# Optimization experiments

Measured on AMD Instinct MI355X. Metric: run time of the kernel, lower is better.

The kernel has to match this reference:

```python
import jax, jax.numpy as jnp
import numpy as np

V, D, H, L, T_MAX = 95, 384, 6, 6, 256
HD = D // H  # 64
FF = 4 * D


def _layernorm(x, scale, bias, eps=1e-5):
    m = jnp.mean(x, axis=-1, keepdims=True)
    v = jnp.var(x, axis=-1, keepdims=True)
    return (x - m) * jax.lax.rsqrt(v + eps) * scale + bias


def setup_inputs() -> dict:
    key = jax.random.key(0)
    ks = iter(jax.random.split(key, 32))
    std = 0.02
    p = {
        "idx": jax.random.randint(next(ks), (128, 256), 0, V, dtype=jnp.int64)
               if jax.config.jax_enable_x64 else
               jax.random.randint(next(ks), (128, 256), 0, V, dtype=jnp.int32),
        "tok_emb": jax.random.normal(next(ks), (V, D), jnp.float32) * std,
        "pos_emb": jax.random.normal(next(ks), (T_MAX, D), jnp.float32) * std,
        # per-layer stacked params [L, ...]
        "ln1_s": jnp.ones((L, D), jnp.float32),
        "ln1_b": jnp.zeros((L, D), jnp.float32),
        "wq": jax.random.normal(next(ks), (L, D, D), jnp.float32) * std,
        "wk": jax.random.normal(next(ks), (L, D, D), jnp.float32) * std,
        "wv": jax.random.normal(next(ks), (L, D, D), jnp.float32) * std,
        "wo": jax.random.normal(next(ks), (L, D, D), jnp.float32) * std,
        "bo": jnp.zeros((L, D), jnp.float32),
        "ln2_s": jnp.ones((L, D), jnp.float32),
        "ln2_b": jnp.zeros((L, D), jnp.float32),
        "w1": jax.random.normal(next(ks), (L, D, FF), jnp.float32) * std,
        "b1": jnp.zeros((L, FF), jnp.float32),
        "w2": jax.random.normal(next(ks), (L, FF, D), jnp.float32) * std,
        "b2": jnp.zeros((L, D), jnp.float32),
        "lnf_s": jnp.ones((D,), jnp.float32),
        "lnf_b": jnp.zeros((D,), jnp.float32),
        "head_w": jax.random.normal(next(ks), (D, V), jnp.float32) * std,
        "head_b": jnp.zeros((V,), jnp.float32),
    }
    return p


def reference(idx, tok_emb, pos_emb, ln1_s, ln1_b, wq, wk, wv, wo, bo,
              ln2_s, ln2_b, w1, b1, w2, b2, lnf_s, lnf_b, head_w, head_b):
    B, T = idx.shape
    x = tok_emb[idx] + pos_emb[:T]  # [B,T,D]
    mask = jnp.tril(jnp.ones((T, T), bool))  # causal
    scale = HD ** -0.5

    def block(x, p):
        s1, b1n, Wq, Wk, Wv, Wo, Bo, s2, b2n, W1, B1, W2, B2 = p
        h = _layernorm(x, s1, b1n)
        q = (h @ Wq).reshape(B, T, H, HD)
        k = (h @ Wk).reshape(B, T, H, HD)
        v = (h @ Wv).reshape(B, T, H, HD)
        scores = jnp.einsum('bqhd,bkhd->bhqk', q, k) * scale
        scores = jnp.where(mask, scores, -jnp.inf)
        wei = jax.nn.softmax(scores, axis=-1)
        attn = jnp.einsum('bhqk,bkhd->bqhd', wei, v).reshape(B, T, D)
        x = x + attn @ Wo + Bo
        h2 = _layernorm(x, s2, b2n)
        x = x + jax.nn.relu(h2 @ W1 + B1) @ W2 + B2
        return x, None

    x, _ = jax.lax.scan(block, x, (ln1_s, ln1_b, wq, wk, wv, wo, bo,
                                   ln2_s, ln2_b, w1, b1, w2, b2))
    logits = _layernorm(x, lnf_s, lnf_b) @ head_w + head_b  # [B,T,V]
    return logits
```

## Files before the change

kernel.cpp:

```cpp
#include <hip/hip_runtime.h>
#include <hip/hip_bf16.h>
#include <cstdint>

#define DEV __device__ __forceinline__

typedef __hip_bfloat16 bf16;
typedef unsigned short u16;
typedef unsigned int u32;
typedef __attribute__((ext_vector_type(8))) short s8v;
typedef __attribute__((ext_vector_type(4))) float f4;

static constexpr int Bn = 128;
static constexpr int Tn = 256;
static constexpr int Dn = 384;
static constexpr int Hn = 6;
static constexpr int HDn = 64;
static constexpr int FFn = 1536;
static constexpr int Vn = 95;
static constexpr int Mn = Bn * 256;

DEV u16 f2b(float f) {
  bf16 h = __float2bfloat16(f);
  return *reinterpret_cast<u16*>(&h);
}
DEV u32 pk2(float a, float b) { return (u32)f2b(a) | ((u32)f2b(b) << 16); }

DEV void gl_lds16(const void* g, void* l) {
  auto gp = (const __attribute__((address_space(1))) u32*)(uintptr_t)g;
  auto lp = (__attribute__((address_space(3))) u32*)(u32)(uintptr_t)l;
  __builtin_amdgcn_global_load_lds(gp, lp, 16, 0, 0);
}

template <int MODE, bool RELU, int NKT, int NT>
__global__ __launch_bounds__(256) void gemm_h(
    const u16* __restrict__ A, const u16* __restrict__ Bw,
    const float* __restrict__ bias, const float* __restrict__ resid,
    void* __restrict__ outp)
{
  constexpr int K = NKT * 64;
  constexpr int N = NT * 16;
  constexpr int nTiles = NT / 8;
  __shared__ __align__(16) u16 As[2][128 * 64];
  const int tid = threadIdx.x;
  const int lane = tid & 63, wave = tid >> 6;
  const int quad = lane >> 4, l16 = lane & 15;
  const int wy = wave >> 1, wx = wave & 1;
  const int blk = blockIdx.x;
  const int xcd = blk & 7, tt = blk >> 3;
  const int nT = tt % nTiles, mT = xcd + 8 * (tt / nTiles);
  const int mBase = mT * 128, nBase = nT * 128;

  f4 acc[4][4] = {};

  int rS[4], cS[4];
#pragma unroll
  for (int i = 0; i < 4; i++) {
    int s = i * 256 + tid;
    rS[i] = s >> 3;
    cS[i] = ((s & 7) ^ (rS[i] & 7)) * 8;
  }

  const u16* Ab = A + (size_t)mBase * K;
  const u16* Bp = Bw + (size_t)((nBase >> 4) + wx * 4) * 512 + lane * 8;

#define STAGEA(buf, kt)                                                       \
  do {                                                                        \
    _Pragma("unroll")                                                         \
    for (int i = 0; i < 4; i++)                                               \
      gl_lds16(Ab + (size_t)rS[i] * K + (kt) + cS[i],                         \
               &As[buf][(i * 256 + wave * 64) * 8]);                          \
  } while (0)

  STAGEA(0, 0);
  const int nk = NKT;
#pragma unroll
  for (int ik = 0; ik < nk; ik++) {
    const int cur = ik & 1;
    asm volatile("s_barrier" ::: "memory");
    s8v bq[8];
    if (ik + 1 < nk) {
      STAGEA(cur ^ 1, (ik + 1) * 64);
#pragma unroll
      for (int ks = 0; ks < 2; ks++)
#pragma unroll
        for (int j = 0; j < 4; j++)
          bq[ks * 4 + j] = *(const s8v*)(Bp + (size_t)(ik * 2 + ks) * (NT * 512) + j * 512);
      asm volatile("s_waitcnt vmcnt(12)" ::: "memory");
    } else {
#pragma unroll
      for (int ks = 0; ks < 2; ks++)
#pragma unroll
        for (int j = 0; j < 4; j++)
          bq[ks * 4 + j] = *(const s8v*)(Bp + (size_t)(ik * 2 + ks) * (NT * 512) + j * 512);
      asm volatile("s_waitcnt vmcnt(8)" ::: "memory");
    }
    asm volatile("s_barrier" ::: "memory");
#pragma unroll
    for (int ks = 0; ks < 2; ks++) {
      s8v af[4];
#pragma unroll
      for (int i = 0; i < 4; i++) {
        int row = wy * 64 + i * 16 + l16;
        int ch = (ks * 4 + quad) ^ (row & 7);
        af[i] = *(const s8v*)&As[cur][row * 64 + ch * 8];
      }
#pragma unroll
      for (int i = 0; i < 4; i++)
#pragma unroll
        for (int j = 0; j < 4; j++)
          acc[i][j] = __builtin_amdgcn_mfma_f32_16x16x32_bf16(af[i], bq[ks * 4 + j], acc[i][j], 0, 0, 0);
    }
  }
#undef STAGEA

  if (MODE == 0) {
    u16* out = (u16*)outp;
#pragma unroll
    for (int j = 0; j < 4; j++) {
      int n = nBase + wx * 64 + j * 16 + l16;
      float bv = bias ? bias[n] : 0.f;
#pragma unroll
      for (int i = 0; i < 4; i++) {
        int m0 = mBase + wy * 64 + i * 16 + quad * 4;
#pragma unroll
        for (int r = 0; r < 4; r++) {
          float v = acc[i][j][r] + bv;
          if (RELU) v = fmaxf(v, 0.f);
          out[(size_t)(m0 + r) * N + n] = f2b(v);
        }
      }
    }
  } else if (MODE == 1) {
    float* out = (float*)outp;
#pragma unroll
    for (int j = 0; j < 4; j++) {
      int n = nBase + wx * 64 + j * 16 + l16;
      float bv = bias[n];
#pragma unroll
      for (int i = 0; i < 4; i++) {
        int m0 = mBase + wy * 64 + i * 16 + quad * 4;
#pragma unroll
        for (int r = 0; r < 4; r++) {
          int m = m0 + r;
          out[(size_t)m * N + n] = resid[(size_t)m * N + n] + acc[i][j][r] + bv;
        }
      }
    }
  } else if (MODE == 3) {
    float* out = (float*)outp;
#pragma unroll
    for (int j = 0; j < 4; j++) {
      int n = nBase + wx * 64 + j * 16 + l16;
      if (n < Vn) {
        float bv = bias[n];
#pragma unroll
        for (int i = 0; i < 4; i++) {
          int m0 = mBase + wy * 64 + i * 16 + quad * 4;
#pragma unroll
          for (int r = 0; r < 4; r++)
            out[(size_t)(m0 + r) * Vn + n] = acc[i][j][r] + bv;
        }
      }
    }
  } else if (MODE == 4) {
    u16* qb = (u16*)outp;
    u16* kb = qb + (size_t)Mn * 384;
    u16* vb = kb + (size_t)Mn * 384;
#pragma unroll
    for (int j = 0; j < 4; j++) {
      int n = nBase + wx * 64 + j * 16 + l16;
      if (n < 768) {
        u16* dst = (n < 384) ? qb : kb;
        int col = (n < 384) ? n : (n - 384);
#pragma unroll
        for (int i = 0; i < 4; i++) {
          int m0 = mBase + wy * 64 + i * 16 + quad * 4;
#pragma unroll
          for (int r = 0; r < 4; r++)
            dst[(size_t)(m0 + r) * 384 + col] = f2b(acc[i][j][r]);
        }
      } else {
        int n7 = n - 768;
        int hh = n7 >> 6, d = n7 & 63;
#pragma unroll
        for (int i = 0; i < 4; i++) {
          int m0 = mBase + wy * 64 + i * 16 + quad * 4;
          int b = m0 >> 8, t0 = m0 & 255;
          uint2 w;
          w.x = pk2(acc[i][j][0], acc[i][j][1]);
          w.y = pk2(acc[i][j][2], acc[i][j][3]);
          *(uint2*)&vb[((b * Hn + hh) * HDn + d) * Tn + t0] = w;
        }
      }
    }
  }
}

__global__ __launch_bounds__(256) void attn_kernel(
    const u16* __restrict__ q, const u16* __restrict__ k,
    const u16* __restrict__ vT, u16* __restrict__ ao)
{
  __shared__ __align__(16) u16 Ps[4][2][16 * 40];
  const int tid = threadIdx.x, lane = tid & 63, wave = tid >> 6;
  const int quad = lane >> 4, l16 = lane & 15;
  const int c4 = blockIdx.x / 768;
  const int bh = blockIdx.x - c4 * 768;
  const int b = bh / Hn, h = bh % Hn;
  const u16* qg = q + (b * Tn) * Dn + h * HDn;
  const u16* kg = k + (b * Tn) * Dn + h * HDn;
  const u16* vg = vT + bh * (HDn * Tn);
  u16* aog = ao + (b * Tn) * Dn + h * HDn;
  const float c1 = 0.125f * 1.44269504f;

  const int qt = (wave & 2) ? ((wave & 1) ? 15 - c4 : 8 + c4)
                            : ((wave & 1) ? 7 - c4 : c4);
  const int qglob = qt * 16 + l16;

  const s8v qf0 = *(const s8v*)&qg[qglob * Dn + quad * 8];
  const s8v qf1 = *(const s8v*)&qg[qglob * Dn + 32 + quad * 8];

  float lsum = 0.f;
  f4 O[4] = {};

  const int nch = qt / 2 + 1;
  for (int c2 = 0; c2 < nch; c2++) {
    const int kk0 = c2 * 32;
    f4 S0 = {0.f, 0.f, 0.f, 0.f}, S1 = S0;
    {
      s8v kf = *(const s8v*)&kg[(kk0 + l16) * Dn + quad * 8];
      S0 = __builtin_amdgcn_mfma_f32_16x16x32_bf16(kf, qf0, S0, 0, 0, 0);
      kf = *(const s8v*)&kg[(kk0 + l16) * Dn + 32 + quad * 8];
      S0 = __builtin_amdgcn_mfma_f32_16x16x32_bf16(kf, qf1, S0, 0, 0, 0);
    }
    if (kk0 + 16 <= qt * 16) {
      s8v kf = *(const s8v*)&kg[(kk0 + 16 + l16) * Dn + quad * 8];
      S1 = __builtin_amdgcn_mfma_f32_16x16x32_bf16(kf, qf0, S1, 0, 0, 0);
      kf = *(const s8v*)&kg[(kk0 + 16 + l16) * Dn + 32 + quad * 8];
      S1 = __builtin_amdgcn_mfma_f32_16x16x32_bf16(kf, qf1, S1, 0, 0, 0);
    }
    const int kkq = kk0 + quad * 4;
    f4 E0, E1;
#pragma unroll
    for (int r = 0; r < 4; r++) {
      E0[r] = (kkq + r <= qglob) ? exp2f(S0[r] * c1) : 0.f;
      E1[r] = (kkq + 16 + r <= qglob) ? exp2f(S1[r] * c1) : 0.f;
      lsum += E0[r] + E1[r];
    }
    u16* prow = &Ps[wave][c2 & 1][l16 * 40];
    uint2 w0, w1;
    w0.x = pk2(E0[0], E0[1]); w0.y = pk2(E0[2], E0[3]);
    w1.x = pk2(E1[0], E1[1]); w1.y = pk2(E1[2], E1[3]);
    *(uint2*)&prow[quad * 4] = w0;
    *(uint2*)&prow[16 + quad * 4] = w1;
    const s8v pf = *(const s8v*)&prow[quad * 8];
#pragma unroll
    for (int dm = 0; dm < 4; dm++) {
      s8v vf = *(const s8v*)&vg[(dm * 16 + l16) * Tn + kk0 + quad * 8];
      O[dm] = __builtin_amdgcn_mfma_f32_16x16x32_bf16(vf, pf, O[dm], 0, 0, 0);
    }
  }

  lsum += __shfl_xor(lsum, 16);
  lsum += __shfl_xor(lsum, 32);
  const float inv = 1.0f / lsum;
#pragma unroll
  for (int dm = 0; dm < 4; dm++) {
    uint2 w;
    w.x = pk2(O[dm][0] * inv, O[dm][1] * inv);
    w.y = pk2(O[dm][2] * inv, O[dm][3] * inv);
    *(uint2*)&aog[qglob * Dn + dm * 16 + quad * 4] = w;
  }
}

__global__ __launch_bounds__(256) void ln_kernel(
    const float* __restrict__ x, const float* __restrict__ sc,
    const float* __restrict__ bi, u16* __restrict__ out)
{
  int tok = blockIdx.x * 4 + (threadIdx.x >> 6);
  int lane = threadIdx.x & 63;
  const float* xr = x + (size_t)tok * Dn;
  float v[6];
  float s = 0.f, sq = 0.f;
#pragma unroll
  for (int i = 0; i < 6; i++) {
    v[i] = xr[lane + 64 * i];
    s += v[i];
    sq += v[i] * v[i];
  }
#pragma unroll
  for (int o = 1; o < 64; o <<= 1) {
    s += __shfl_xor(s, o);
    sq += __shfl_xor(sq, o);
  }
  float mean = s * (1.f / 384.f);
  float var = sq * (1.f / 384.f) - mean * mean;
  float inv = rsqrtf(var + 1e-5f);
  u16* orow = out + (size_t)tok * Dn;
#pragma unroll
  for (int i = 0; i < 6; i++) {
    int c = lane + 64 * i;
    orow[c] = f2b((v[i] - mean) * inv * sc[c] + bi[c]);
  }
}

__global__ __launch_bounds__(256) void embed_kernel(
    const int* __restrict__ idx, const float* __restrict__ tok,
    const float* __restrict__ pos, float* __restrict__ x)
{
  int i = blockIdx.x * 256 + threadIdx.x;
  int m = i / 96, c = (i - m * 96) * 4;
  int t = m & (Tn - 1);
  const float4 tv = *(const float4*)&tok[idx[m] * Dn + c];
  const float4 pv = *(const float4*)&pos[t * Dn + c];
  float4 r;
  r.x = tv.x + pv.x; r.y = tv.y + pv.y; r.z = tv.z + pv.z; r.w = tv.w + pv.w;
  *(float4*)&x[m * Dn + c] = r;
}

__global__ __launch_bounds__(256) void tcvt_frag(
    const float* __restrict__ src, u16* __restrict__ dst,
    int K, int C, int NTsub, int NTtot, int ntoff, int total)
{
  int t = blockIdx.x * 256 + threadIdx.x;
  if (t >= total) return;
  int j8 = t & 7;
  int lane = (t >> 3) & 63;
  int rest = t >> 9;
  int nt = rest % NTsub;
  int lkc = rest / NTsub;
  int KC = K >> 5;
  int kc = lkc % KC;
  int l = lkc / KC;
  int quad = lane >> 4, l16 = lane & 15;
  int k = kc * 32 + quad * 8 + j8;
  int n = nt * 16 + l16;
  float v = (n < C) ? src[((size_t)l * K + k) * C + n] : 0.f;
  dst[((size_t)(l * KC + kc) * NTtot + ntoff + nt) * 512 + lane * 8 + j8] = f2b(v);
}

extern "C" void kernel_launch(void* const* d_in, const int* in_sizes, int n_in,
                              void* d_out, int out_size, void* d_ws, size_t ws_size,
                              hipStream_t stream)
{
  (void)in_sizes; (void)n_in; (void)out_size;
  const int*   idx     = (const int*)d_in[0];
  const float* tok_emb = (const float*)d_in[1];
  const float* pos_emb = (const float*)d_in[2];
  const float* ln1_s   = (const float*)d_in[3];
  const float* ln1_b   = (const float*)d_in[4];
  const float* wq      = (const float*)d_in[5];
  const float* wk      = (const float*)d_in[6];
  const float* wv      = (const float*)d_in[7];
  const float* wo      = (const float*)d_in[8];
  const float* bo      = (const float*)d_in[9];
  const float* ln2_s   = (const float*)d_in[10];
  const float* ln2_b   = (const float*)d_in[11];
  const float* w1      = (const float*)d_in[12];
  const float* b1      = (const float*)d_in[13];
  const float* w2      = (const float*)d_in[14];
  const float* b2      = (const float*)d_in[15];
  const float* lnf_s   = (const float*)d_in[16];
  const float* lnf_b   = (const float*)d_in[17];
  const float* head_w  = (const float*)d_in[18];
  const float* head_b  = (const float*)d_in[19];
  float* out = (float*)d_out;

  char* ws = (char*)d_ws;
  float* x  = (float*)(ws + 0);
  u16*   h  = (u16*)(ws + 50331648);
  u16*   qb = (u16*)(ws + 75497472);
  u16*   kb = (u16*)(ws + 100663296);
  u16*   vb = (u16*)(ws + 125829120);
  u16*   ab = (u16*)(ws + 150994944);
  u16*   f1 = qb;
  u16* qkvT = (u16*)(ws + 176160768);
  u16* woT  = qkvT + 6 * 442368;
  u16* w1T  = woT + 6 * 147456;
  u16* w2T  = w1T + 6 * 589824;
  u16* hdT  = w2T + 6 * 589824;
  if (ws_size < (size_t)197492736) return;

  int tot = 6 * 384 * 384;
  tcvt_frag<<<(tot + 255) / 256, 256, 0, stream>>>(wq, qkvT, 384, 384, 24, 72, 0, tot);
  tcvt_frag<<<(tot + 255) / 256, 256, 0, stream>>>(wk, qkvT, 384, 384, 24, 72, 24, tot);
  tcvt_frag<<<(tot + 255) / 256, 256, 0, stream>>>(wv, qkvT, 384, 384, 24, 72, 48, tot);
  tcvt_frag<<<(tot + 255) / 256, 256, 0, stream>>>(wo, woT, 384, 384, 24, 24, 0, tot);
  tot = 6 * 384 * 1536;
  tcvt_frag<<<(tot + 255) / 256, 256, 0, stream>>>(w1, w1T, 384, 1536, 96, 96, 0, tot);
  tcvt_frag<<<(tot + 255) / 256, 256, 0, stream>>>(w2, w2T, 1536, 384, 24, 24, 0, tot);
  tot = 384 * 128;
  tcvt_frag<<<(tot + 255) / 256, 256, 0, stream>>>(head_w, hdT, 384, 95, 8, 8, 0, tot);

  embed_kernel<<<(Mn * 96) / 256, 256, 0, stream>>>(idx, tok_emb, pos_emb, x);

  for (int l = 0; l < 6; l++) {
    ln_kernel<<<Mn / 4, 256, 0, stream>>>(x, ln1_s + l * Dn, ln1_b + l * Dn, h);
    gemm_h<4, false, 6, 72><<<2304, 256, 0, stream>>>(h, qkvT + l * 442368, nullptr, nullptr, qb);
    attn_kernel<<<Bn * Hn * 4, 256, 0, stream>>>(qb, kb, vb, ab);
    gemm_h<1, false, 6, 24><<<768, 256, 0, stream>>>(ab, woT + l * 147456, bo + l * Dn, x, x);
    ln_kernel<<<Mn / 4, 256, 0, stream>>>(x, ln2_s + l * Dn, ln2_b + l * Dn, h);
    gemm_h<0, true, 6, 96><<<3072, 256, 0, stream>>>(h, w1T + l * 589824, b1 + l * FFn, nullptr, f1);
    gemm_h<1, false, 24, 24><<<768, 256, 0, stream>>>(f1, w2T + l * 589824, b2 + l * Dn, x, x);
  }
  ln_kernel<<<Mn / 4, 256, 0, stream>>>(x, lnf_s, lnf_b, h);
  gemm_h<3, false, 6, 8><<<256, 256, 0, stream>>>(h, hdT, head_b, nullptr, out);
}
```

Measured before the change: 1.656 ms.

## Add 64-row GEMM tile for N=384 residual GEMMs and vectorize epilogue stores

Adds a gemm_m64 kernel with 64x128 tiles for the Wo and W2 projections (N=384). The launch grid doubles from 768 to 1536 blocks so the GPU's compute units are better filled. It swaps the MFMA operand order so each lane holds four consecutive columns, which lets the epilogue use float4 residual, bias and output accesses, and the FFN1 bf16 output uses packed 8-byte stores. The cost is less A/B reuse per block and more B-fragment loads overall.

```diff
diff --git a/kernel.cpp b/kernel.cpp
--- a/kernel.cpp
+++ b/kernel.cpp
@@ -40,6 +40,7 @@
   constexpr int K = NKT * 64;
   constexpr int N = NT * 16;
   constexpr int nTiles = NT / 8;
+  constexpr bool SW = (MODE == 0);
   __shared__ __align__(16) u16 As[2][128 * 64];
   const int tid = threadIdx.x;
   const int lane = tid & 63, wave = tid >> 6;
@@ -107,8 +108,12 @@
 #pragma unroll
       for (int i = 0; i < 4; i++)
 #pragma unroll
-        for (int j = 0; j < 4; j++)
-          acc[i][j] = __builtin_amdgcn_mfma_f32_16x16x32_bf16(af[i], bq[ks * 4 + j], acc[i][j], 0, 0, 0);
+        for (int j = 0; j < 4; j++) {
+          if (SW)
+            acc[i][j] = __builtin_amdgcn_mfma_f32_16x16x32_bf16(bq[ks * 4 + j], af[i], acc[i][j], 0, 0, 0);
+          else
+            acc[i][j] = __builtin_amdgcn_mfma_f32_16x16x32_bf16(af[i], bq[ks * 4 + j], acc[i][j], 0, 0, 0);
+        }
     }
   }
 #undef STAGEA
@@ -116,34 +121,22 @@
   if (MODE == 0) {
     u16* out = (u16*)outp;
 #pragma unroll
-    for (int j = 0; j < 4; j++) {
-      int n = nBase + wx * 64 + j * 16 + l16;
-      float bv = bias ? bias[n] : 0.f;
-#pragma unroll
-      for (int i = 0; i < 4; i++) {
-        int m0 = mBase + wy * 64 + i * 16 + quad * 4;
-#pragma unroll
-        for (int r = 0; r < 4; r++) {
-          float v = acc[i][j][r] + bv;
-          if (RELU) v = fmaxf(v, 0.f);
-          out[(size_t)(m0 + r) * N + n] = f2b(v);
+    for (int i = 0; i < 4; i++) {
+      int m = mBase + wy * 64 + i * 16 + l16;
+#pragma unroll
+      for (int j = 0; j < 4; j++) {
+        int n0 = nBase + wx * 64 + j * 16 + quad * 4;
+        float4 bv = bias ? *(const float4*)&bias[n0] : make_float4(0.f, 0.f, 0.f, 0.f);
+        float v0 = acc[i][j][0] + bv.x, v1 = acc[i][j][1] + bv.y;
+        float v2 = acc[i][j][2] + bv.z, v3 = acc[i][j][3] + bv.w;
+        if (RELU) {
+          v0 = fmaxf(v0, 0.f); v1 = fmaxf(v1, 0.f);
+          v2 = fmaxf(v2, 0.f); v3 = fmaxf(v3, 0.f);
         }
-      }
-    }
-  } else if (MODE == 1) {
-    float* out = (float*)outp;
-#pragma unroll
-    for (int j = 0; j < 4; j++) {
-      int n = nBase + wx * 64 + j * 16 + l16;
-      float bv = bias[n];
-#pragma unroll
-      for (int i = 0; i < 4; i++) {
-        int m0 = mBase + wy * 64 + i * 16 + quad * 4;
-#pragma unroll
-        for (int r = 0; r < 4; r++) {
-          int m = m0 + r;
-          out[(size_t)m * N + n] = resid[(size_t)m * N + n] + acc[i][j][r] + bv;
-        }
+        uint2 w;
+        w.x = pk2(v0, v1);
+        w.y = pk2(v2, v3);
+        *(uint2*)&out[(size_t)m * N + n0] = w;
       }
     }
   } else if (MODE == 3) {
@@ -192,6 +185,105 @@
           *(uint2*)&vb[((b * Hn + hh) * HDn + d) * Tn + t0] = w;
         }
       }
+    }
+  }
+}
+
+template <int NKT>
+__global__ __launch_bounds__(256) void gemm_m64(
+    const u16* __restrict__ A, const u16* __restrict__ Bw,
+    const float* __restrict__ bias, const float* __restrict__ resid,
+    float* __restrict__ outp)
+{
+  constexpr int K = NKT * 64;
+  constexpr int N = 384;
+  constexpr int NT = 24;
+  __shared__ __align__(16) u16 As[2][64 * 64];
+  const int tid = threadIdx.x;
+  const int lane = tid & 63, wave = tid >> 6;
+  const int quad = lane >> 4, l16 = lane & 15;
+  const int wy = wave >> 1, wx = wave & 1;
+  const int blk = blockIdx.x;
+  const int xcd = blk & 7, tt = blk >> 3;
+  const int nT = tt % 3, mT = xcd + 8 * (tt / 3);
+  const int mBase = mT * 64, nBase = nT * 128;
+
+  f4 acc[2][4] = {};
+
+  int rS[2], cS[2];
+#pragma unroll
+  for (int i = 0; i < 2; i++) {
+    int s = i * 256 + tid;
+    rS[i] = s >> 3;
+    cS[i] = ((s & 7) ^ (rS[i] & 7)) * 8;
+  }
+
+  const u16* Ab = A + (size_t)mBase * K;
+  const u16* Bp = Bw + (size_t)((nBase >> 4) + wx * 4) * 512 + lane * 8;
+
+#define STAGEA64(buf, kt)                                                     \
+  do {                                                                        \
+    _Pragma("unroll")                                                         \
+    for (int i = 0; i < 2; i++)                                               \
+      gl_lds16(Ab + (size_t)rS[i] * K + (kt) + cS[i],                         \
+               &As[buf][(i * 256 + wave * 64) * 8]);                          \
+  } while (0)
+
+  STAGEA64(0, 0);
+#pragma unroll
+  for (int ik = 0; ik < NKT; ik++) {
+    const int cur = ik & 1;
+    asm volatile("s_barrier" ::: "memory");
+    s8v bq[8];
+    if (ik + 1 < NKT) {
+      STAGEA64(cur ^ 1, (ik + 1) * 64);
+#pragma unroll
+      for (int ks = 0; ks < 2; ks++)
+#pragma unroll
+        for (int j = 0; j < 4; j++)
+          bq[ks * 4 + j] = *(const s8v*)(Bp + (size_t)(ik * 2 + ks) * (NT * 512) + j * 512);
+      asm volatile("s_waitcnt vmcnt(10)" ::: "memory");
+    } else {
+#pragma unroll
+      for (int ks = 0; ks < 2; ks++)
+#pragma unroll
+        for (int j = 0; j < 4; j++)
+          bq[ks * 4 + j] = *(const s8v*)(Bp + (size_t)(ik * 2 + ks) * (NT * 512) + j * 512);
+      asm volatile("s_waitcnt vmcnt(8)" ::: "memory");
+    }
+    asm volatile("s_barrier" ::: "memory");
+#pragma unroll
+    for (int ks = 0; ks < 2; ks++) {
+      s8v af[2];
+#pragma unroll
+      for (int i = 0; i < 2; i++) {
+        int row = wy * 32 + i * 16 + l16;
+        int ch = (ks * 4 + quad) ^ (row & 7);
+        af[i] = *(const s8v*)&As[cur][row * 64 + ch * 8];
+      }
+#pragma unroll
+      for (int i = 0; i < 2; i++)
+#pragma unroll
+        for (int j = 0; j < 4; j++)
+          acc[i][j] = __builtin_amdgcn_mfma_f32_16x16x32_bf16(bq[ks * 4 + j], af[i], acc[i][j], 0, 0, 0);
+    }
+  }
+#undef STAGEA64
+
+#pragma unroll
+  for (int i = 0; i < 2; i++) {
+    int m = mBase + wy * 32 + i * 16 + l16;
+#pragma unroll
+    for (int j = 0; j < 4; j++) {
+      int n0 = nBase + wx * 64 + j * 16 + quad * 4;
+      float4 rv = *(const float4*)&resid[(size_t)m * N + n0];
+      float4 bv = *(const float4*)&bias[n0];
+      float4 o;
+      o.x = rv.x + acc[i][j][0] + bv.x;
+      o.y = rv.y + acc[i][j][1] + bv.y;
+      o.z = rv.z + acc[i][j][2] + bv.z;
+      o.w = rv.w + acc[i][j][3] + bv.w;
+      *(float4*)&outp[(size_t)m * N + n0] = o;
     }
   }
 }
@@ -397,10 +489,10 @@
     ln_kernel<<<Mn / 4, 256, 0, stream>>>(x, ln1_s + l * Dn, ln1_b + l * Dn, h);
     gemm_h<4, false, 6, 72><<<2304, 256, 0, stream>>>(h, qkvT + l * 442368, nullptr, nullptr, qb);
     attn_kernel<<<Bn * Hn * 4, 256, 0, stream>>>(qb, kb, vb, ab);
-    gemm_h<1, false, 6, 24><<<768, 256, 0, stream>>>(ab, woT + l * 147456, bo + l * Dn, x, x);
+    gemm_m64<6><<<1536, 256, 0, stream>>>(ab, woT + l * 147456, bo + l * Dn, x, x);
     ln_kernel<<<Mn / 4, 256, 0, stream>>>(x, ln2_s + l * Dn, ln2_b + l * Dn, h);
     gemm_h<0, true, 6, 96><<<3072, 256, 0, stream>>>(h, w1T + l * 589824, b1 + l * FFn, nullptr, f1);
-    gemm_h<1, false, 24, 24><<<768, 256, 0, stream>>>(f1, w2T + l * 589824, b2 + l * Dn, x, x);
+    gemm_m64<24><<<1536, 256, 0, stream>>>(f1, w2T + l * 589824, b2 + l * Dn, x, x);
   }
   ln_kernel<<<Mn / 4, 256, 0, stream>>>(x, lnf_s, lnf_b, h);
   gemm_h<3, false, 6, 8><<<256, 256, 0, stream>>>(h, hdT, head_b, nullptr, out);
```

New measurement: 1.793 ms. 1.08x slower.
